# Optimization experiments

Hardware: AMD Instinct MI355X
Metric: run time of the kernel (lower is better)

Reference implementation:

```python
import jax, jax.numpy as jnp
import numpy as np

B, T, D = 2, 2048, 1024
HV, HK = 16, 8
DK, DV = 64, 64
K_DIM = HK * DK          # 512
V_DIM = HV * DV          # 1024
CONV_DIM = 2 * K_DIM + V_DIM  # 2048
KS = 4                   # short-conv kernel size
EPS = 1e-6               # rms_norm_eps / l2norm eps


def setup_inputs() -> dict:
    key = jax.random.key(0)
    ks = jax.random.split(key, 9)
    g = lambda k, shape, sc: (jax.random.normal(k, shape, jnp.float32) * sc)
    return {
        "hidden_states": g(ks[0], (B, T, D), 1.0),
        "W_qkv": g(ks[1], (D, CONV_DIM), 0.02),
        "W_z": g(ks[2], (D, V_DIM), 0.02),
        "W_b": g(ks[3], (D, HV), 0.02),
        "W_a": g(ks[4], (D, HV), 0.02),
        "dt_bias": jnp.ones((HV,), jnp.float32),
        "A_log": jnp.log(jax.random.uniform(ks[5], (HV,), jnp.float32, 1e-3, 16.0)),
        "conv_w": g(ks[6], (CONV_DIM, KS), 0.2),
        "norm_w": jnp.ones((DV,), jnp.float32),
        "W_out": g(ks[7], (V_DIM, D), 0.02),
    }


def _causal_conv_silu(x, w):
    # depthwise causal conv1d over time, followed by SiLU (FLA ShortConvolution default)
    # x: [B,T,C], w: [C,KS]
    xp = jnp.pad(x, ((0, 0), (KS - 1, 0), (0, 0)))
    y = sum(xp[:, i:i + x.shape[1], :] * w[:, i] for i in range(KS))
    return jax.nn.silu(y)


def _l2norm(x):
    return x * jax.lax.rsqrt(jnp.sum(x * x, -1, keepdims=True) + EPS)


def _forward(hidden_states, W_qkv, W_z, W_b, W_a, dt_bias, A_log, conv_w, norm_w, W_out):
    b_, t_ = hidden_states.shape[:2]
    mixed_qkv = hidden_states @ W_qkv                       # [B,T,conv_dim]
    z = (hidden_states @ W_z).reshape(b_, t_, HV, DV)       # gate branch
    beta = jax.nn.sigmoid(hidden_states @ W_b)              # [B,T,HV]
    g = -jnp.exp(A_log) * jax.nn.softplus(hidden_states @ W_a + dt_bias)  # [B,T,HV]

    mixed_qkv = _causal_conv_silu(mixed_qkv, conv_w)
    q, k, v = jnp.split(mixed_qkv, [K_DIM, 2 * K_DIM], axis=-1)
    q = q.reshape(b_, t_, HK, DK)
    k = k.reshape(b_, t_, HK, DK)
    v = v.reshape(b_, t_, HV, DV)
    # GQA expansion of q/k to the value-head count
    rep = HV // HK
    q = jnp.repeat(q, rep, axis=2)
    k = jnp.repeat(k, rep, axis=2)
    # l2-norm on q/k in kernel; q additionally scaled by 1/sqrt(dk)
    q = _l2norm(q) * (DK ** -0.5)
    k = _l2norm(k)

    # gated delta-rule recurrence over time (state S: [B,HV,DK,DV])
    qT = q.transpose(1, 0, 2, 3)
    kT = k.transpose(1, 0, 2, 3)
    vT = v.transpose(1, 0, 2, 3)
    gT = g.transpose(1, 0, 2)
    bT = beta.transpose(1, 0, 2)

    def step(S, xs):
        q_t, k_t, v_t, g_t, b_t = xs
        S = S * jnp.exp(g_t)[..., None, None]
        kv = jnp.einsum('bhk,bhkv->bhv', k_t, S)
        S = S + jnp.einsum('bhk,bhv->bhkv', k_t, (v_t - kv) * b_t[..., None])
        o_t = jnp.einsum('bhk,bhkv->bhv', q_t, S)
        return S, o_t

    S0 = jnp.zeros((b_, HV, DK, DV), jnp.float32)
    _, oT = jax.lax.scan(step, S0, (qT, kT, vT, gT, bT))
    o = oT.transpose(1, 0, 2, 3)                            # [B,T,HV,DV]

    # gated RMSNorm: rmsnorm(o) * weight * silu(z)
    var = jnp.mean(o * o, axis=-1, keepdims=True)
    o = o * jax.lax.rsqrt(var + EPS) * norm_w * jax.nn.silu(z)

    return o.reshape(b_, t_, V_DIM) @ W_out


def reference(hidden_states, W_qkv, W_z, W_b, W_a, dt_bias, A_log, conv_w, norm_w, W_out):
    return _forward(hidden_states, W_qkv, W_z, W_b, W_a, dt_bias, A_log, conv_w, norm_w, W_out)
```

## Files before the change

kernel.cpp:

```cpp
#include <hip/hip_runtime.h>
#include <hip/hip_bf16.h>


typedef unsigned short u16;
typedef float f32x4 __attribute__((ext_vector_type(4)));
typedef short bf16x8 __attribute__((ext_vector_type(8)));
typedef u16 u16x4 __attribute__((ext_vector_type(4)));
typedef const __attribute__((address_space(1))) void* gptr_t;
typedef __attribute__((address_space(3))) void* lptr_t;

#define B_    2
#define T_    2048
#define HV_   16
#define HK_   8
#define NC_   32
#define BT_   4096
#define QKVZ_ 3072
#define NCOL_ 3200

__device__ __forceinline__ u16 f2bf(float f) {
  return __builtin_bit_cast(u16, __float2bfloat16(f));
}
__device__ __forceinline__ float bf2f(u16 u) {
  return __bfloat162float(__builtin_bit_cast(__hip_bfloat16, u));
}
__device__ __forceinline__ float sigm(float x) { return 1.f / (1.f + __expf(-x)); }

__global__ __launch_bounds__(256) void k_cast_hs(const float* __restrict__ in,
                                                 u16* __restrict__ out) {
  int i = (blockIdx.x * 256 + threadIdx.x) * 4;
  float4 v = *(const float4*)(in + i);
  u16x4 o; o.x = f2bf(v.x); o.y = f2bf(v.y); o.z = f2bf(v.z); o.w = f2bf(v.w);
  *(u16x4*)(out + i) = o;
}

__global__ __launch_bounds__(256) void k_tcast(const float* __restrict__ src,
                                               u16* __restrict__ dst, int R, int C) {
  __shared__ float tile[32][33];
  int c0 = blockIdx.x * 32, r0 = blockIdx.y * 32;
  int cx = threadIdx.x & 31, ry = threadIdx.x >> 5;
#pragma unroll
  for (int j = 0; j < 4; ++j)
    tile[ry * 4 + j][cx] = src[(long)(r0 + ry * 4 + j) * C + c0 + cx];
  __syncthreads();
#pragma unroll
  for (int j = 0; j < 4; ++j)
    dst[(long)(c0 + ry * 4 + j) * R + r0 + cx] = f2bf(tile[cx][ry * 4 + j]);
}

__global__ __launch_bounds__(256) void k_wcatT(const float* __restrict__ Wqkv,
                                               const float* __restrict__ Wz,
                                               const float* __restrict__ Wb,
                                               const float* __restrict__ Wa,
                                               u16* __restrict__ dst) {
  __shared__ float tile[32][33];
  int n0 = blockIdx.x * 32, k0 = blockIdx.y * 32;
  int cx = threadIdx.x & 31, ry = threadIdx.x >> 5;
#pragma unroll
  for (int j = 0; j < 4; ++j) {
    int kk = k0 + ry * 4 + j;
    int n = n0 + cx;
    float v;
    if (n < 2048)      v = Wqkv[(long)kk * 2048 + n];
    else if (n < 3072) v = Wz[(long)kk * 1024 + (n - 2048)];
    else if (n < 3088) v = Wb[kk * 16 + (n - 3072)];
    else if (n < 3104) v = Wa[kk * 16 + (n - 3088)];
    else               v = 0.f;
    tile[ry * 4 + j][cx] = v;
  }
  __syncthreads();
#pragma unroll
  for (int j = 0; j < 4; ++j)
    dst[(long)(n0 + ry * 4 + j) * 1024 + k0 + cx] = f2bf(tile[cx][ry * 4 + j]);
}

__global__ __launch_bounds__(256) void k_gemm(const u16* __restrict__ A,
                                              const u16* __restrict__ Bt,
                                              u16* __restrict__ C0,
                                              float* __restrict__ C1,
                                              int M, int N, int K, int mode) {
  __shared__ u16 As[128 * 64];
  __shared__ u16 Bs[128 * 64];
  int tid = threadIdx.x;
  int wid = tid >> 6, lane = tid & 63;
  int row0 = blockIdx.y * 128, col0 = blockIdx.x * 128;
  int wr = wid >> 1, wc = wid & 1;
  f32x4 acc[4][4];
#pragma unroll
  for (int m = 0; m < 4; ++m)
#pragma unroll
    for (int n = 0; n < 4; ++n) acc[m][n] = (f32x4){0.f, 0.f, 0.f, 0.f};

  int srow = lane >> 3;
  int skoff = (lane & 7) * 8;

  for (int k0 = 0; k0 < K; k0 += 64) {
#pragma unroll
    for (int it = 0; it < 4; ++it) {
      int seg = wid * 4 + it;
      int r = seg * 8 + srow;
      const u16* gA = A + (long)(row0 + r) * K + k0 + skoff;
      const u16* gB = Bt + (long)(col0 + r) * K + k0 + skoff;
      __builtin_amdgcn_global_load_lds((gptr_t)gA, (lptr_t)(As + seg * 512), 16, 0, 0);
      __builtin_amdgcn_global_load_lds((gptr_t)gB, (lptr_t)(Bs + seg * 512), 16, 0, 0);
    }
    asm volatile("s_waitcnt vmcnt(0)" ::: "memory");
    __syncthreads();
#pragma unroll
    for (int ks = 0; ks < 2; ++ks) {
      bf16x8 af[4], bfr[4];
      int kk = ks * 32 + (lane >> 4) * 8;
      int rA = wr * 64 + (lane & 15);
      int rB = wc * 64 + (lane & 15);
#pragma unroll
      for (int m = 0; m < 4; ++m) af[m] = *(const bf16x8*)(As + (rA + m * 16) * 64 + kk);
#pragma unroll
      for (int n = 0; n < 4; ++n) bfr[n] = *(const bf16x8*)(Bs + (rB + n * 16) * 64 + kk);
#pragma unroll
      for (int m = 0; m < 4; ++m)
#pragma unroll
        for (int n = 0; n < 4; ++n)
          acc[m][n] = __builtin_amdgcn_mfma_f32_16x16x32_bf16(af[m], bfr[n], acc[m][n], 0, 0, 0);
    }
    __syncthreads();
  }
#pragma unroll
  for (int m = 0; m < 4; ++m)
#pragma unroll
    for (int n = 0; n < 4; ++n)
#pragma unroll
      for (int r = 0; r < 4; ++r) {
        int row = row0 + wr * 64 + m * 16 + (lane >> 4) * 4 + r;
        int col = col0 + wc * 64 + n * 16 + (lane & 15);
        float v = acc[m][n][r];
        if (mode == 0) {
          if (col < QKVZ_) C0[(long)row * QKVZ_ + col] = f2bf(v);
          else             C1[(long)row * 128 + (col - QKVZ_)] = v;
        } else {
          C1[(long)row * N + col] = v;
        }
      }
}

__global__ __launch_bounds__(64) void k_conv(const u16* __restrict__ qkvz,
                                             const float* __restrict__ ba,
                                             const float* __restrict__ convw,
                                             const float* __restrict__ Alog,
                                             const float* __restrict__ dtb,
                                             u16* __restrict__ qn, u16* __restrict__ kn,
                                             u16* __restrict__ vb,
                                             float* __restrict__ beta, float* __restrict__ gb) {
  int bt = blockIdx.x;
  int t = bt & 2047;
  int l = threadIdx.x;
  long rb = (long)bt * QKVZ_;
#pragma unroll 1
  for (int j = 0; j < 32; ++j) {
    int c = j * 64 + l;
    float4 w = *(const float4*)(convw + c * 4);
    float a = 0.f;
#pragma unroll
    for (int d = 0; d < 4; ++d) {
      int tt = t - 3 + d;
      float x = (tt >= 0) ? bf2f(qkvz[rb + (long)(tt - t) * QKVZ_ + c]) : 0.f;
      a += x * ((const float*)&w)[d];
    }
    float y = a * sigm(a);
    if (j < 16) {
      float ss = y * y;
#pragma unroll
      for (int m = 1; m < 64; m <<= 1) ss += __shfl_xor(ss, m);
      float sc = rsqrtf(ss + 1e-6f);
      if (j < 8) qn[((long)bt * 8 + j) * 64 + l] = f2bf(y * sc * 0.125f);
      else       kn[((long)bt * 8 + (j - 8)) * 64 + l] = f2bf(y * sc);
    } else {
      vb[((long)bt * 16 + (j - 16)) * 64 + l] = f2bf(y);
    }
  }
  if (l < 16) {
    float xb = ba[(long)bt * 128 + l];
    beta[bt * 16 + l] = sigm(xb);
    float xa = ba[(long)bt * 128 + 16 + l] + dtb[l];
    float sp = (xa > 20.f) ? xa : log1pf(__expf(xa));
    gb[bt * 16 + l] = -__expf(Alog[l]) * sp;
  }
}

__global__ __launch_bounds__(256) void k_cpk2(const u16* __restrict__ qn,
                                              const u16* __restrict__ kn,
                                              const u16* __restrict__ vb,
                                              const float* __restrict__ beta,
                                              const float* __restrict__ gb,
                                              float* __restrict__ Gbuf,
                                              u16* __restrict__ TKTb,
                                              u16* __restrict__ WlTb, u16* __restrict__ MTb,
                                              u16* __restrict__ Pb, u16* __restrict__ Bb) {
  int c = blockIdx.x, hv = blockIdx.y, b = blockIdx.z;
  int hk = hv >> 1;
  int bh = b * HV_ + hv;
  int tid = threadIdx.x;
  int wv = tid >> 6, lane = tid & 63;
  int frow = lane & 15, fk = (lane >> 4) * 8;

  __shared__ __align__(16) char smem[78848];
  u16* Ks   = (u16*)smem;
  u16* Qs   = (u16*)(smem + 9216);
  u16* Ktt  = Qs;
  u16* As_  = (u16*)(smem + 18432);
  u16* RHSt = (u16*)(smem + 27648);
  u16* Xt   = (u16*)(smem + 46080);
  u16* T4   = (u16*)(smem + 64512);
  u16* Yl   = (u16*)(smem + 68608);
  __shared__ float Gl[64];
  __shared__ float Bl[64];

  long tbase = (long)b * T_ + c * 64;
  long tile = ((long)bh * NC_ + c) * 4096;

  if (tid < 64) {
    Gl[tid] = gb[(tbase + tid) * HV_ + hv];
    Bl[tid] = beta[(tbase + tid) * HV_ + hv];
  }
  if (tid == 0) {
    float s = 0.f;
    for (int i = 0; i < 64; ++i) { s += Gl[i]; Gl[i] = s; }
  }
  if (tid < 64) Gbuf[((long)bh * NC_ + c) * 64 + tid] = Gl[tid];
  for (int e = tid; e < 4608; e += 256) ((float*)Xt)[e] = 0.f;
  for (int e = tid; e < 2560; e += 256) ((float*)Yl)[e] = 0.f;
  for (int e = tid; e < 4096; e += 256) {
    int i = e >> 6, k = e & 63;
    Ks[i * 72 + k] = kn[(tbase + i) * 512 + hk * 64 + k];
    Qs[i * 72 + k] = qn[(tbase + i) * 512 + hk * 64 + k];
  }
  __syncthreads();

  {
    bf16x8 aKs[2];
#pragma unroll
    for (int ks = 0; ks < 2; ++ks)
      aKs[ks] = *(const bf16x8*)&Ks[(wv * 16 + frow) * 72 + ks * 32 + fk];
    f32x4 accM[4], accA[4];
#pragma unroll
    for (int nt = 0; nt < 4; ++nt) { accM[nt] = (f32x4){0,0,0,0}; accA[nt] = (f32x4){0,0,0,0}; }
#pragma unroll
    for (int ks = 0; ks < 2; ++ks) {
#pragma unroll
      for (int nt = 0; nt < 4; ++nt) {
        bf16x8 bq = *(const bf16x8*)&Qs[(nt * 16 + frow) * 72 + ks * 32 + fk];
        bf16x8 bk = *(const bf16x8*)&Ks[(nt * 16 + frow) * 72 + ks * 32 + fk];
        accM[nt] = __builtin_amdgcn_mfma_f32_16x16x32_bf16(aKs[ks], bq, accM[nt], 0, 0, 0);
        accA[nt] = __builtin_amdgcn_mfma_f32_16x16x32_bf16(aKs[ks], bk, accA[nt], 0, 0, 0);
      }
    }
#pragma unroll
    for (int nt = 0; nt < 4; ++nt) {
      int i = nt * 16 + frow;
#pragma unroll
      for (int r = 0; r < 4; ++r) {
        int s = wv * 16 + (lane >> 4) * 4 + r;
        float val = (s <= i) ? accM[nt][r] * __expf(Gl[i] - Gl[s]) : 0.f;
        MTb[tile + s * 64 + i] = f2bf(val);
      }
    }
#pragma unroll
    for (int nt = 0; nt < 4; ++nt) {
      int s = nt * 16 + frow;
#pragma unroll
      for (int r = 0; r < 4; ++r) {
        int i = wv * 16 + (lane >> 4) * 4 + r;
        float val = (s < i) ? Bl[i] * __expf(Gl[i] - Gl[s]) * accA[nt][r] : 0.f;
        As_[i * 72 + s] = f2bf(val);
      }
    }
  }

  for (int e = tid; e < 4096; e += 256) {
    int i = e >> 6, v = e & 63;
    RHSt[v * 72 + i] = f2bf(Bl[i] * bf2f(vb[(tbase + i) * 1024 + hv * 64 + v]));
  }
  for (int e = tid; e < 4096; e += 256) {
    int i = e >> 6, k = e & 63;
    RHSt[(64 + k) * 72 + i] = f2bf(Bl[i] * __expf(Gl[i]) * bf2f(Ks[i * 72 + k]));
  }
  __syncthreads();

  {
    if (lane < 16) {
      int cc = lane;
      float Tc[16];
#pragma unroll
      for (int j = 0; j < 16; ++j) Tc[j] = (j == cc) ? 1.f : 0.f;
#pragma unroll
      for (int s = 0; s < 15; ++s)
#pragma unroll
        for (int i = s + 1; i < 16; ++i) {
          float a = bf2f(As_[(wv * 16 + i) * 72 + wv * 16 + s]);
          Tc[i] -= a * Tc[s];
        }
#pragma unroll
      for (int i = 0; i < 16; ++i) T4[(wv * 16 + i) * 32 + cc] = f2bf(Tc[i]);
    } else if (lane < 32) {
      int c2 = lane - 16;
#pragma unroll
      for (int i = 0; i < 16; ++i) T4[(wv * 16 + i) * 32 + 16 + c2] = 0;
    }
  }
  __syncthreads();

#pragma unroll 1
  for (int bb = 0; bb < 4; ++bb) {
    f32x4 uacc[2];
    uacc[0] = (f32x4){0,0,0,0}; uacc[1] = (f32x4){0,0,0,0};
#pragma unroll
    for (int ks = 0; ks < 2; ++ks) {
      bf16x8 bfr = *(const bf16x8*)&As_[(bb * 16 + frow) * 72 + ks * 32 + fk];
#pragma unroll
      for (int mt = 0; mt < 2; ++mt) {
        bf16x8 aa = *(const bf16x8*)&Xt[((wv * 2 + mt) * 16 + frow) * 72 + ks * 32 + fk];
        uacc[mt] = __builtin_amdgcn_mfma_f32_16x16x32_bf16(aa, bfr, uacc[mt], 0, 0, 0);
      }
    }
#pragma unroll
    for (int mt = 0; mt < 2; ++mt)
#pragma unroll
      for (int r = 0; r < 4; ++r) {
        int vr = (wv * 2 + mt) * 16 + (lane >> 4) * 4 + r;
        float y = bf2f(RHSt[vr * 72 + bb * 16 + frow]) - uacc[mt][r];
        Yl[vr * 40 + frow] = f2bf(y);
      }
    __syncthreads();
    {
      bf16x8 tb = *(const bf16x8*)&T4[(bb * 16 + frow) * 32 + fk];
      f32x4 zacc[2];
      zacc[0] = (f32x4){0,0,0,0}; zacc[1] = (f32x4){0,0,0,0};
#pragma unroll
      for (int mt = 0; mt < 2; ++mt) {
        bf16x8 aa = *(const bf16x8*)&Yl[((wv * 2 + mt) * 16 + frow) * 40 + fk];
        zacc[mt] = __builtin_amdgcn_mfma_f32_16x16x32_bf16(aa, tb, zacc[mt], 0, 0, 0);
      }
#pragma unroll
      for (int mt = 0; mt < 2; ++mt)
#pragma unroll
        for (int r = 0; r < 4; ++r) {
          int vr = (wv * 2 + mt) * 16 + (lane >> 4) * 4 + r;
          Xt[vr * 72 + bb * 16 + frow] = f2bf(zacc[mt][r]);
        }
    }
    __syncthreads();
  }

  float gend = Gl[63];
  for (int e = tid; e < 4096; e += 256) {
    int i = e >> 6, r = e & 63;
    Ktt[r * 72 + i] = f2bf(__expf(gend - Gl[i]) * bf2f(Ks[i * 72 + r]));
  }
#pragma unroll
  for (int t8 = 0; t8 < 2; ++t8) {
    int seg = tid + t8 * 256;
    int row = seg >> 2, s4 = (seg & 3) * 16;
    bf16x8 x0 = *(const bf16x8*)&Xt[row * 72 + s4];
    bf16x8 x1 = *(const bf16x8*)&Xt[row * 72 + s4 + 8];
    u16* dst = (row < 64) ? (WlTb + tile + row * 64 + s4)
                          : (TKTb + tile + (long)(row - 64) * 64 + s4);
    *(bf16x8*)dst = x0;
    *(bf16x8*)(dst + 8) = x1;
  }
  __syncthreads();

  {
    f32x4 acc[4];
#pragma unroll
    for (int nt = 0; nt < 4; ++nt) acc[nt] = (f32x4){0,0,0,0};
#pragma unroll
    for (int ks = 0; ks < 2; ++ks) {
      bf16x8 aa = *(const bf16x8*)&Ktt[(wv * 16 + frow) * 72 + ks * 32 + fk];
#pragma unroll
      for (int nt = 0; nt < 4; ++nt) {
        bf16x8 bfr = *(const bf16x8*)&Xt[(nt * 16 + frow) * 72 + ks * 32 + fk];
        acc[nt] = __builtin_amdgcn_mfma_f32_16x16x32_bf16(aa, bfr, acc[nt], 0, 0, 0);
      }
    }
#pragma unroll
    for (int nt = 0; nt < 4; ++nt) {
      int v = nt * 16 + frow;
#pragma unroll
      for (int r = 0; r < 4; ++r) {
        int rr = wv * 16 + (lane >> 4) * 4 + r;
        Bb[tile + rr * 64 + v] = f2bf(acc[nt][r]);
      }
    }
  }
  {
    f32x4 acc[4];
#pragma unroll
    for (int nt = 0; nt < 4; ++nt) acc[nt] = (f32x4){0,0,0,0};
#pragma unroll
    for (int ks = 0; ks < 2; ++ks) {
      bf16x8 aa = *(const bf16x8*)&Xt[(64 + wv * 16 + frow) * 72 + ks * 32 + fk];
#pragma unroll
      for (int nt = 0; nt < 4; ++nt) {
        bf16x8 bfr = *(const bf16x8*)&Ktt[(nt * 16 + frow) * 72 + ks * 32 + fk];
        acc[nt] = __builtin_amdgcn_mfma_f32_16x16x32_bf16(aa, bfr, acc[nt], 0, 0, 0);
      }
    }
#pragma unroll
    for (int nt = 0; nt < 4; ++nt) {
      int rr = nt * 16 + frow;
#pragma unroll
      for (int r = 0; r < 4; ++r) {
        int k2 = wv * 16 + (lane >> 4) * 4 + r;
        Pb[tile + k2 * 64 + rr] = f2bf(acc[nt][r]);
      }
    }
  }
}

__global__ __launch_bounds__(256) void k_seq2(const u16* __restrict__ Pb,
                                              const u16* __restrict__ Bb,
                                              const float* __restrict__ Gbuf,
                                              u16* __restrict__ Stb) {
  int vblk = blockIdx.x, bh = blockIdx.y;
  int tid = threadIdx.x;
  __shared__ u16 Abf[2][4096];
  __shared__ u16 Bbf[2][512];
  __shared__ float S_lds[64][10];
  __shared__ float gam[NC_];
  int i_ = tid & 63, vg = tid >> 6;
  int wv = tid >> 6, ln = tid & 63;
  if (tid < NC_) gam[tid] = __expf(Gbuf[((long)bh * NC_ + tid) * 64 + 63]);
  for (int e = tid; e < 640; e += 256) ((float*)S_lds)[e] = 0.f;
  float a0 = 0.f, a1 = 0.f;
  {
    long tl = (long)bh * NC_ * 4096;
    const u16* gA = Pb + tl + wv * 512 + ln * 8;
    __builtin_amdgcn_global_load_lds((gptr_t)gA, (lptr_t)&Abf[0][wv * 512], 16, 0, 0);
    __builtin_amdgcn_global_load_lds((gptr_t)(gA + 2048), (lptr_t)&Abf[0][2048 + wv * 512], 16, 0, 0);
    int ii = tid >> 2, vp = tid & 3;
    const u16* gB = Bb + tl + ii * 64 + vblk * 8 + vp * 2;
    __builtin_amdgcn_global_load_lds((gptr_t)gB, (lptr_t)&Bbf[0][wv * 128], 4, 0, 0);
  }
  for (int c = 0; c < NC_; ++c) {
    int cur = c & 1;
    asm volatile("s_waitcnt vmcnt(0)" ::: "memory");
    __syncthreads();
    if (c + 1 < NC_) {
      long tl = ((long)bh * NC_ + c + 1) * 4096;
      const u16* gA = Pb + tl + wv * 512 + ln * 8;
      __builtin_amdgcn_global_load_lds((gptr_t)gA, (lptr_t)&Abf[cur ^ 1][wv * 512], 16, 0, 0);
      __builtin_amdgcn_global_load_lds((gptr_t)(gA + 2048), (lptr_t)&Abf[cur ^ 1][2048 + wv * 512], 16, 0, 0);
      int ii = tid >> 2, vp = tid & 3;
      const u16* gB = Bb + tl + ii * 64 + vblk * 8 + vp * 2;
      __builtin_amdgcn_global_load_lds((gptr_t)gB, (lptr_t)&Bbf[cur ^ 1][wv * 128], 4, 0, 0);
    }
    {
      long stile = ((long)bh * NC_ + c) * 4096;
      int v0 = vblk * 8 + vg * 2;
      Stb[stile + (long)v0 * 64 + i_] = f2bf(a0);
      Stb[stile + (long)(v0 + 1) * 64 + i_] = f2bf(a1);
    }
    float g = gam[c];
    float n0 = 0.f, n1 = 0.f;
#pragma unroll 8
    for (int k = 0; k < 64; ++k) {
      float p = bf2f(Abf[cur][k * 64 + i_]);
      float2 sv = *(const float2*)&S_lds[k][vg * 2];
      n0 += p * sv.x;
      n1 += p * sv.y;
    }
    float b0 = bf2f(Bbf[cur][i_ * 8 + vg * 2]);
    float b1 = bf2f(Bbf[cur][i_ * 8 + vg * 2 + 1]);
    a0 = g * a0 - n0 + b0;
    a1 = g * a1 - n1 + b1;
    __syncthreads();
    S_lds[i_][vg * 2] = a0;
    S_lds[i_][vg * 2 + 1] = a1;
  }
}

__global__ __launch_bounds__(256) void k_ok2(const u16* __restrict__ MTb,
                                             const u16* __restrict__ TKTb,
                                             const u16* __restrict__ WlTb,
                                             const u16* __restrict__ Stb,
                                             const u16* __restrict__ qn,
                                             const float* __restrict__ Gbuf,
                                             float* __restrict__ O) {
  int c = blockIdx.x, hv = blockIdx.y, b = blockIdx.z;
  int bh = b * HV_ + hv, hk = hv >> 1;
  int tid = threadIdx.x;
  __shared__ float TKt[64][68];
  __shared__ float Ss[64][68];
  __shared__ float Ws[64][68];
  __shared__ float Qt[64][68];
  __shared__ float Gl[64];
  long tile = ((long)bh * NC_ + c) * 4096;
  long tbase = (long)b * T_ + c * 64;
  if (tid < 64) Gl[tid] = Gbuf[((long)bh * NC_ + c) * 64 + tid];
  __syncthreads();
  for (int e = tid; e < 4096; e += 256)
    TKt[e >> 6][e & 63] = bf2f(TKTb[tile + e]);
  for (int e = tid; e < 4096; e += 256) {
    int i = e >> 6, k = e & 63;
    Qt[k][i] = __expf(Gl[i]) * bf2f(qn[(tbase + i) * 512 + hk * 64 + k]);
  }
  for (int e = tid; e < 4096; e += 256) {
    int v = e >> 6, x = e & 63;
    Ss[x][v] = bf2f(Stb[tile + e]);
    Ws[x][v] = bf2f(WlTb[tile + e]);
  }
  __syncthreads();
  int tx = tid & 15, ty = tid >> 4;
  int i0 = ty * 4, v0 = tx * 4;
  float w[4][4];
#pragma unroll
  for (int r = 0; r < 4; ++r) *(f32x4*)w[r] = *(const f32x4*)&Ws[i0 + r][v0];
  for (int k = 0; k < 64; ++k) {
    f32x4 tk = *(const f32x4*)&TKt[k][i0];
    f32x4 sv = *(const f32x4*)&Ss[k][v0];
#pragma unroll
    for (int r = 0; r < 4; ++r)
#pragma unroll
      for (int q = 0; q < 4; ++q) w[r][q] -= tk[r] * sv[q];
  }
  __syncthreads();
#pragma unroll
  for (int r = 0; r < 4; ++r) *(f32x4*)&Ws[i0 + r][v0] = *(const f32x4*)w[r];
  for (int e = tid; e < 4096; e += 256)
    TKt[e >> 6][e & 63] = bf2f(MTb[tile + e]);
  __syncthreads();
  float o[4][4] = {};
  for (int s = 0; s < 64; ++s) {
    f32x4 mv = *(const f32x4*)&TKt[s][i0];
    f32x4 wv = *(const f32x4*)&Ws[s][v0];
#pragma unroll
    for (int r = 0; r < 4; ++r)
#pragma unroll
      for (int q = 0; q < 4; ++q) o[r][q] += mv[r] * wv[q];
  }
  for (int k = 0; k < 64; ++k) {
    f32x4 qv = *(const f32x4*)&Qt[k][i0];
    f32x4 sv = *(const f32x4*)&Ss[k][v0];
#pragma unroll
    for (int r = 0; r < 4; ++r)
#pragma unroll
      for (int q = 0; q < 4; ++q) o[r][q] += qv[r] * sv[q];
  }
#pragma unroll
  for (int r = 0; r < 4; ++r) {
    float4 o4 = make_float4(o[r][0], o[r][1], o[r][2], o[r][3]);
    *(float4*)&O[((tbase + i0 + r) * HV_ + hv) * 64 + v0] = o4;
  }
}

__global__ __launch_bounds__(256) void k_rms(const float* __restrict__ O,
                                             const u16* __restrict__ qkvz,
                                             const float* __restrict__ normw,
                                             u16* __restrict__ on) {
  int bt = blockIdx.x;
  int tid = threadIdx.x;
  __shared__ float ps[256];
  __shared__ float rstd[16];
  float4 o4 = *(const float4*)&O[(long)bt * 1024 + tid * 4];
  ps[tid] = o4.x * o4.x + o4.y * o4.y + o4.z * o4.z + o4.w * o4.w;
  __syncthreads();
  if (tid < 16) {
    float s = 0.f;
#pragma unroll
    for (int u = 0; u < 16; ++u) s += ps[tid * 16 + u];
    rstd[tid] = rsqrtf(s * (1.f / 64.f) + 1e-6f);
  }
  __syncthreads();
  float rs = rstd[tid >> 4];
  u16x4 ov;
#pragma unroll
  for (int j = 0; j < 4; ++j) {
    int idx = tid * 4 + j;
    float z = bf2f(qkvz[(long)bt * QKVZ_ + 2048 + idx]);
    float val = ((const float*)&o4)[j] * rs * normw[idx & 63] * (z * sigm(z));
    ((u16*)&ov)[j] = f2bf(val);
  }
  *(u16x4*)(on + (long)bt * 1024 + tid * 4) = ov;
}

extern "C" void kernel_launch(void* const* d_in, const int* in_sizes, int n_in,
                              void* d_out, int out_size, void* d_ws, size_t ws_size,
                              hipStream_t stream) {
  const float* hs    = (const float*)d_in[0];
  const float* Wqkv  = (const float*)d_in[1];
  const float* Wz    = (const float*)d_in[2];
  const float* Wb    = (const float*)d_in[3];
  const float* Wa    = (const float*)d_in[4];
  const float* dtb   = (const float*)d_in[5];
  const float* Alog  = (const float*)d_in[6];
  const float* convw = (const float*)d_in[7];
  const float* normw = (const float*)d_in[8];
  const float* Wout  = (const float*)d_in[9];
  float* out = (float*)d_out;

  char* p = (char*)d_ws;
  auto take = [&](size_t bytes) {
    char* q = p;
    p += (bytes + 255) & ~(size_t)255;
    return (void*)q;
  };
  u16*   qkvz  = (u16*)take((size_t)BT_ * QKVZ_ * 2);
  float* ba    = (float*)take((size_t)BT_ * 128 * 4);
  u16*   hsb   = (u16*)take((size_t)BT_ * 1024 * 2);
  u16*   wcatT = (u16*)take((size_t)NCOL_ * 1024 * 2);
  u16*   woutT = (u16*)take((size_t)1024 * 1024 * 2);
  u16*   qn    = (u16*)take((size_t)BT_ * 512 * 2);
  u16*   kn    = (u16*)take((size_t)BT_ * 512 * 2);
  u16*   vbuf  = (u16*)take((size_t)BT_ * 1024 * 2);
  float* beta  = (float*)take((size_t)BT_ * 16 * 4);
  float* gbuf  = (float*)take((size_t)BT_ * 16 * 4);
  float* Gcum  = (float*)take((size_t)1024 * 64 * 4);
  u16*   TKTb  = (u16*)take((size_t)1024 * 4096 * 2);
  u16*   WlTb  = (u16*)take((size_t)1024 * 4096 * 2);
  u16*   MTb   = (u16*)take((size_t)1024 * 4096 * 2);
  u16*   Pb    = (u16*)take((size_t)1024 * 4096 * 2);
  u16*   Bb    = (u16*)take((size_t)1024 * 4096 * 2);
  u16*   Stb   = (u16*)take((size_t)1024 * 4096 * 2);
  float* Obuf  = (float*)take((size_t)BT_ * 1024 * 4);
  u16*   onb   = (u16*)take((size_t)BT_ * 1024 * 2);

  k_cast_hs<<<dim3(4096), dim3(256), 0, stream>>>(hs, hsb);
  k_wcatT<<<dim3(100, 32), dim3(256), 0, stream>>>(Wqkv, Wz, Wb, Wa, wcatT);
  k_tcast<<<dim3(32, 32), dim3(256), 0, stream>>>(Wout, woutT, 1024, 1024);
  k_gemm<<<dim3(25, 32), dim3(256), 0, stream>>>(hsb, wcatT, qkvz, ba, 4096, NCOL_, 1024, 0);
  k_conv<<<dim3(4096), dim3(64), 0, stream>>>(qkvz, ba, convw, Alog, dtb, qn, kn, vbuf, beta, gbuf);
  k_cpk2<<<dim3(32, 16, 2), dim3(256), 0, stream>>>(qn, kn, vbuf, beta, gbuf, Gcum, TKTb, WlTb, MTb, Pb, Bb);
  k_seq2<<<dim3(8, 32), dim3(256), 0, stream>>>(Pb, Bb, Gcum, Stb);
  k_ok2<<<dim3(32, 16, 2), dim3(256), 0, stream>>>(MTb, TKTb, WlTb, Stb, qn, Gcum, Obuf);
  k_rms<<<dim3(4096), dim3(256), 0, stream>>>(Obuf, qkvz, normw, onb);
  k_gemm<<<dim3(8, 32), dim3(256), 0, stream>>>(onb, woutT, (u16*)nullptr, out, 4096, 1024, 1024, 1);
}
```

Before: 363.0 us.

## Add pipelined 256x256 input GEMM, vectorize conv, move chunk output to MFMA

Replaces the input projection GEMM with a 512-thread 256x256-tile kernel. It uses a 4-stage global_load_lds pipeline with swizzled LDS and setprio around the MFMAs, and pads the weight columns to 3328. The conv kernel now handles 8 channels per thread with vector bf16 loads, and its l2norm reduction needs only 3 shuffles. The chunk output kernel drops its fp32 scalar outer products for bf16 MFMA, with the M/TK intermediate layouts changed to match. The risks are bf16 rounding of the intermediate W and Q tiles and lower occupancy in the big GEMM.

Result: faster. 291.9 us (-19.6%).

```diff
diff --git a/kernel.cpp b/kernel.cpp
--- a/kernel.cpp
+++ b/kernel.cpp
@@ -16,7 +16,7 @@
 #define NC_   32
 #define BT_   4096
 #define QKVZ_ 3072
-#define NCOL_ 3200
+#define NPAD_ 3328
 
 __device__ __forceinline__ u16 f2bf(float f) {
   return __builtin_bit_cast(u16, __float2bfloat16(f));
@@ -74,11 +74,101 @@
     dst[(long)(n0 + ry * 4 + j) * 1024 + k0 + cx] = f2bf(tile[cx][ry * 4 + j]);
 }
 
+__global__ __launch_bounds__(512, 1) void k_g1(const u16* __restrict__ A,
+                                               const u16* __restrict__ Bt,
+                                               u16* __restrict__ C0,
+                                               float* __restrict__ C1) {
+  extern __shared__ u16 smem[];
+  const int K = 1024;
+  int tid = threadIdx.x;
+  int wv = tid >> 6, lane = tid & 63;
+  int wm = wv >> 2, wn = wv & 3;
+  int frow = lane & 15, kq = lane >> 4;
+  long row0 = blockIdx.y * 256, col0 = blockIdx.x * 256;
+
+  f32x4 acc[8][4];
+#pragma unroll
+  for (int m = 0; m < 8; ++m)
+#pragma unroll
+    for (int n = 0; n < 4; ++n) acc[m][n] = (f32x4){0.f, 0.f, 0.f, 0.f};
+
+  int lr = lane >> 2;
+  int kc_src = ((lane & 3) - (lane >> 3)) & 3;
+
+  auto stage = [&](int ts) {
+#pragma unroll
+    for (int op = 0; op < 2; ++op) {
+      u16* base = smem + op * 32768 + (ts & 3) * 8192;
+      const u16* gsrc = op ? Bt : A;
+      long grow0 = op ? col0 : row0;
+#pragma unroll
+      for (int it = 0; it < 2; ++it) {
+        int seg = wv * 2 + it;
+        const u16* g = gsrc + (grow0 + seg * 16 + lr) * K + ts * 32 + kc_src * 8;
+        __builtin_amdgcn_global_load_lds((gptr_t)g, (lptr_t)(base + seg * 512), 16, 0, 0);
+      }
+    }
+  };
+
+  auto section = [&](int h) {
+    const char* Ab = (const char*)(smem + (h & 3) * 8192);
+    const char* Bb = (const char*)(smem + 32768 + (h & 3) * 8192);
+    bf16x8 af[8], bfr[4];
+#pragma unroll
+    for (int mt = 0; mt < 8; ++mt) {
+      int R = wm * 128 + mt * 16 + frow;
+      af[mt] = *(const bf16x8*)(Ab + R * 64 + (((kq + (R >> 1)) & 3) << 4));
+    }
+#pragma unroll
+    for (int nt = 0; nt < 4; ++nt) {
+      int R = wn * 64 + nt * 16 + frow;
+      bfr[nt] = *(const bf16x8*)(Bb + R * 64 + (((kq + (R >> 1)) & 3) << 4));
+    }
+    __builtin_amdgcn_s_setprio(1);
+#pragma unroll
+    for (int mt = 0; mt < 8; ++mt)
+#pragma unroll
+      for (int nt = 0; nt < 4; ++nt)
+        acc[mt][nt] = __builtin_amdgcn_mfma_f32_16x16x32_bf16(af[mt], bfr[nt], acc[mt][nt], 0, 0, 0);
+    __builtin_amdgcn_s_setprio(0);
+  };
+
+  stage(0); stage(1); stage(2);
+#pragma unroll 1
+  for (int h = 0; h < 29; ++h) {
+    asm volatile("s_waitcnt vmcnt(8)" ::: "memory");
+    __syncthreads();
+    stage(h + 3);
+    section(h);
+  }
+  asm volatile("s_waitcnt vmcnt(8)" ::: "memory");
+  __syncthreads();
+  section(29);
+  asm volatile("s_waitcnt vmcnt(4)" ::: "memory");
+  __syncthreads();
+  section(30);
+  asm volatile("s_waitcnt vmcnt(0)" ::: "memory");
+  __syncthreads();
+  section(31);
+
+#pragma unroll
+  for (int m = 0; m < 8; ++m)
+#pragma unroll
+    for (int n = 0; n < 4; ++n)
+#pragma unroll
+      for (int r = 0; r < 4; ++r) {
+        long row = row0 + wm * 128 + m * 16 + kq * 4 + r;
+        long col = col0 + wn * 64 + n * 16 + frow;
+        float v = acc[m][n][r];
+        if (col < QKVZ_)      C0[row * QKVZ_ + col] = f2bf(v);
+        else if (col < 3200)  C1[row * 128 + (col - QKVZ_)] = v;
+      }
+}
+
 __global__ __launch_bounds__(256) void k_gemm(const u16* __restrict__ A,
                                               const u16* __restrict__ Bt,
-                                              u16* __restrict__ C0,
                                               float* __restrict__ C1,
-                                              int M, int N, int K, int mode) {
+                                              int M, int N, int K) {
   __shared__ u16 As[128 * 64];
   __shared__ u16 Bs[128 * 64];
   int tid = threadIdx.x;
@@ -90,10 +180,8 @@
   for (int m = 0; m < 4; ++m)
 #pragma unroll
     for (int n = 0; n < 4; ++n) acc[m][n] = (f32x4){0.f, 0.f, 0.f, 0.f};
-
   int srow = lane >> 3;
   int skoff = (lane & 7) * 8;
-
   for (int k0 = 0; k0 < K; k0 += 64) {
 #pragma unroll
     for (int it = 0; it < 4; ++it) {
@@ -132,57 +220,68 @@
       for (int r = 0; r < 4; ++r) {
         int row = row0 + wr * 64 + m * 16 + (lane >> 4) * 4 + r;
         int col = col0 + wc * 64 + n * 16 + (lane & 15);
-        float v = acc[m][n][r];
-        if (mode == 0) {
-          if (col < QKVZ_) C0[(long)row * QKVZ_ + col] = f2bf(v);
-          else             C1[(long)row * 128 + (col - QKVZ_)] = v;
-        } else {
-          C1[(long)row * N + col] = v;
-        }
-      }
-}
-
-__global__ __launch_bounds__(64) void k_conv(const u16* __restrict__ qkvz,
-                                             const float* __restrict__ ba,
-                                             const float* __restrict__ convw,
-                                             const float* __restrict__ Alog,
-                                             const float* __restrict__ dtb,
-                                             u16* __restrict__ qn, u16* __restrict__ kn,
-                                             u16* __restrict__ vb,
-                                             float* __restrict__ beta, float* __restrict__ gb) {
+        C1[(long)row * N + col] = acc[m][n][r];
+      }
+}
+
+__global__ __launch_bounds__(256) void k_conv(const u16* __restrict__ qkvz,
+                                              const float* __restrict__ ba,
+                                              const float* __restrict__ convw,
+                                              const float* __restrict__ Alog,
+                                              const float* __restrict__ dtb,
+                                              u16* __restrict__ qn, u16* __restrict__ kn,
+                                              u16* __restrict__ vb,
+                                              float* __restrict__ beta, float* __restrict__ gb) {
   int bt = blockIdx.x;
   int t = bt & 2047;
-  int l = threadIdx.x;
+  int g = threadIdx.x;
+  int c = g * 8;
   long rb = (long)bt * QKVZ_;
-#pragma unroll 1
-  for (int j = 0; j < 32; ++j) {
-    int c = j * 64 + l;
-    float4 w = *(const float4*)(convw + c * 4);
+  bf16x8 x[4];
+#pragma unroll
+  for (int d = 0; d < 4; ++d) {
+    int tt = t - 3 + d;
+    if (tt >= 0) x[d] = *(const bf16x8*)(qkvz + rb + (long)(d - 3) * QKVZ_ + c);
+    else         x[d] = (bf16x8){0, 0, 0, 0, 0, 0, 0, 0};
+  }
+  float y[8];
+#pragma unroll
+  for (int j = 0; j < 8; ++j) {
+    float4 w4 = *(const float4*)(convw + (c + j) * 4);
     float a = 0.f;
 #pragma unroll
     for (int d = 0; d < 4; ++d) {
       int tt = t - 3 + d;
-      float x = (tt >= 0) ? bf2f(qkvz[rb + (long)(tt - t) * QKVZ_ + c]) : 0.f;
-      a += x * ((const float*)&w)[d];
-    }
-    float y = a * sigm(a);
-    if (j < 16) {
-      float ss = y * y;
-#pragma unroll
-      for (int m = 1; m < 64; m <<= 1) ss += __shfl_xor(ss, m);
-      float sc = rsqrtf(ss + 1e-6f);
-      if (j < 8) qn[((long)bt * 8 + j) * 64 + l] = f2bf(y * sc * 0.125f);
-      else       kn[((long)bt * 8 + (j - 8)) * 64 + l] = f2bf(y * sc);
-    } else {
-      vb[((long)bt * 16 + (j - 16)) * 64 + l] = f2bf(y);
-    }
-  }
-  if (l < 16) {
-    float xb = ba[(long)bt * 128 + l];
-    beta[bt * 16 + l] = sigm(xb);
-    float xa = ba[(long)bt * 128 + 16 + l] + dtb[l];
+      float xv = (tt >= 0) ? bf2f((u16)x[d][j]) : 0.f;
+      a += xv * ((const float*)&w4)[d];
+    }
+    y[j] = a * sigm(a);
+  }
+  bf16x8 o;
+  if (g < 128) {
+    float ss = 0.f;
+#pragma unroll
+    for (int j = 0; j < 8; ++j) ss += y[j] * y[j];
+    ss += __shfl_xor(ss, 1);
+    ss += __shfl_xor(ss, 2);
+    ss += __shfl_xor(ss, 4);
+    float sc = rsqrtf(ss + 1e-6f);
+    if (g < 64) sc *= 0.125f;
+#pragma unroll
+    for (int j = 0; j < 8; ++j) ((u16*)&o)[j] = f2bf(y[j] * sc);
+    if (g < 64) *(bf16x8*)(qn + (long)bt * 512 + c) = o;
+    else        *(bf16x8*)(kn + (long)bt * 512 + (c - 512)) = o;
+  } else {
+#pragma unroll
+    for (int j = 0; j < 8; ++j) ((u16*)&o)[j] = f2bf(y[j]);
+    *(bf16x8*)(vb + (long)bt * 1024 + (c - 1024)) = o;
+  }
+  if (g < 16) {
+    float xb = ba[(long)bt * 128 + g];
+    beta[bt * 16 + g] = sigm(xb);
+    float xa = ba[(long)bt * 128 + 16 + g] + dtb[g];
     float sp = (xa > 20.f) ? xa : log1pf(__expf(xa));
-    gb[bt * 16 + l] = -__expf(Alog[l]) * sp;
+    gb[bt * 16 + g] = -__expf(Alog[g]) * sp;
   }
 }
 
@@ -192,8 +291,8 @@
                                               const float* __restrict__ beta,
                                               const float* __restrict__ gb,
                                               float* __restrict__ Gbuf,
-                                              u16* __restrict__ TKTb,
-                                              u16* __restrict__ WlTb, u16* __restrict__ MTb,
+                                              u16* __restrict__ TKb,
+                                              u16* __restrict__ WlTb, u16* __restrict__ Mb,
                                               u16* __restrict__ Pb, u16* __restrict__ Bb) {
   int c = blockIdx.x, hv = blockIdx.y, b = blockIdx.z;
   int hk = hv >> 1;
@@ -236,10 +335,12 @@
   __syncthreads();
 
   {
-    bf16x8 aKs[2];
-#pragma unroll
-    for (int ks = 0; ks < 2; ++ks)
+    bf16x8 aKs[2], aQs[2];
+#pragma unroll
+    for (int ks = 0; ks < 2; ++ks) {
       aKs[ks] = *(const bf16x8*)&Ks[(wv * 16 + frow) * 72 + ks * 32 + fk];
+      aQs[ks] = *(const bf16x8*)&Qs[(wv * 16 + frow) * 72 + ks * 32 + fk];
+    }
     f32x4 accM[4], accA[4];
 #pragma unroll
     for (int nt = 0; nt < 4; ++nt) { accM[nt] = (f32x4){0,0,0,0}; accA[nt] = (f32x4){0,0,0,0}; }
@@ -247,20 +348,19 @@
     for (int ks = 0; ks < 2; ++ks) {
 #pragma unroll
       for (int nt = 0; nt < 4; ++nt) {
-        bf16x8 bq = *(const bf16x8*)&Qs[(nt * 16 + frow) * 72 + ks * 32 + fk];
         bf16x8 bk = *(const bf16x8*)&Ks[(nt * 16 + frow) * 72 + ks * 32 + fk];
-        accM[nt] = __builtin_amdgcn_mfma_f32_16x16x32_bf16(aKs[ks], bq, accM[nt], 0, 0, 0);
+        accM[nt] = __builtin_amdgcn_mfma_f32_16x16x32_bf16(aQs[ks], bk, accM[nt], 0, 0, 0);
         accA[nt] = __builtin_amdgcn_mfma_f32_16x16x32_bf16(aKs[ks], bk, accA[nt], 0, 0, 0);
       }
     }
 #pragma unroll
     for (int nt = 0; nt < 4; ++nt) {
-      int i = nt * 16 + frow;
-#pragma unroll
-      for (int r = 0; r < 4; ++r) {
-        int s = wv * 16 + (lane >> 4) * 4 + r;
+      int s = nt * 16 + frow;
+#pragma unroll
+      for (int r = 0; r < 4; ++r) {
+        int i = wv * 16 + (lane >> 4) * 4 + r;
         float val = (s <= i) ? accM[nt][r] * __expf(Gl[i] - Gl[s]) : 0.f;
-        MTb[tile + s * 64 + i] = f2bf(val);
+        Mb[tile + i * 64 + s] = f2bf(val);
       }
     }
 #pragma unroll
@@ -356,15 +456,17 @@
     Ktt[r * 72 + i] = f2bf(__expf(gend - Gl[i]) * bf2f(Ks[i * 72 + r]));
   }
 #pragma unroll
-  for (int t8 = 0; t8 < 2; ++t8) {
-    int seg = tid + t8 * 256;
+  for (int t8 = 0; t8 < 1; ++t8) {
+    int seg = tid;
     int row = seg >> 2, s4 = (seg & 3) * 16;
     bf16x8 x0 = *(const bf16x8*)&Xt[row * 72 + s4];
     bf16x8 x1 = *(const bf16x8*)&Xt[row * 72 + s4 + 8];
-    u16* dst = (row < 64) ? (WlTb + tile + row * 64 + s4)
-                          : (TKTb + tile + (long)(row - 64) * 64 + s4);
-    *(bf16x8*)dst = x0;
-    *(bf16x8*)(dst + 8) = x1;
+    *(bf16x8*)(WlTb + tile + row * 64 + s4) = x0;
+    *(bf16x8*)(WlTb + tile + row * 64 + s4 + 8) = x1;
+  }
+  for (int e = tid; e < 4096; e += 256) {
+    int i = e >> 6, k = e & 63;
+    TKb[tile + e] = Xt[(64 + k) * 72 + i];
   }
   __syncthreads();
 
@@ -478,8 +580,8 @@
   }
 }
 
-__global__ __launch_bounds__(256) void k_ok2(const u16* __restrict__ MTb,
-                                             const u16* __restrict__ TKTb,
+__global__ __launch_bounds__(256) void k_ok3(const u16* __restrict__ Mb,
+                                             const u16* __restrict__ TKb,
                                              const u16* __restrict__ WlTb,
                                              const u16* __restrict__ Stb,
                                              const u16* __restrict__ qn,
@@ -488,67 +590,84 @@
   int c = blockIdx.x, hv = blockIdx.y, b = blockIdx.z;
   int bh = b * HV_ + hv, hk = hv >> 1;
   int tid = threadIdx.x;
-  __shared__ float TKt[64][68];
-  __shared__ float Ss[64][68];
-  __shared__ float Ws[64][68];
-  __shared__ float Qt[64][68];
+  int wv = tid >> 6, lane = tid & 63;
+  int frow = lane & 15, fk = (lane >> 4) * 8;
+  __shared__ __align__(16) u16 St[64 * 72];
+  __shared__ __align__(16) u16 TKr[64 * 72];
+  __shared__ __align__(16) u16 Wl_[64 * 72];
+  __shared__ __align__(16) u16 Qh[64 * 72];
   __shared__ float Gl[64];
   long tile = ((long)bh * NC_ + c) * 4096;
   long tbase = (long)b * T_ + c * 64;
   if (tid < 64) Gl[tid] = Gbuf[((long)bh * NC_ + c) * 64 + tid];
-  __syncthreads();
-  for (int e = tid; e < 4096; e += 256)
-    TKt[e >> 6][e & 63] = bf2f(TKTb[tile + e]);
+  bf16x8 mreg[2];
+#pragma unroll
+  for (int j = 0; j < 2; ++j) mreg[j] = *(const bf16x8*)(Mb + tile + tid * 16 + j * 8);
+  __syncthreads();
   for (int e = tid; e < 4096; e += 256) {
-    int i = e >> 6, k = e & 63;
-    Qt[k][i] = __expf(Gl[i]) * bf2f(qn[(tbase + i) * 512 + hk * 64 + k]);
-  }
-  for (int e = tid; e < 4096; e += 256) {
-    int v = e >> 6, x = e & 63;
-    Ss[x][v] = bf2f(Stb[tile + e]);
-    Ws[x][v] = bf2f(WlTb[tile + e]);
-  }
-  __syncthreads();
-  int tx = tid & 15, ty = tid >> 4;
-  int i0 = ty * 4, v0 = tx * 4;
-  float w[4][4];
-#pragma unroll
-  for (int r = 0; r < 4; ++r) *(f32x4*)w[r] = *(const f32x4*)&Ws[i0 + r][v0];
-  for (int k = 0; k < 64; ++k) {
-    f32x4 tk = *(const f32x4*)&TKt[k][i0];
-    f32x4 sv = *(const f32x4*)&Ss[k][v0];
-#pragma unroll
-    for (int r = 0; r < 4; ++r)
-#pragma unroll
-      for (int q = 0; q < 4; ++q) w[r][q] -= tk[r] * sv[q];
-  }
-  __syncthreads();
-#pragma unroll
-  for (int r = 0; r < 4; ++r) *(f32x4*)&Ws[i0 + r][v0] = *(const f32x4*)w[r];
-  for (int e = tid; e < 4096; e += 256)
-    TKt[e >> 6][e & 63] = bf2f(MTb[tile + e]);
-  __syncthreads();
-  float o[4][4] = {};
-  for (int s = 0; s < 64; ++s) {
-    f32x4 mv = *(const f32x4*)&TKt[s][i0];
-    f32x4 wv = *(const f32x4*)&Ws[s][v0];
-#pragma unroll
-    for (int r = 0; r < 4; ++r)
-#pragma unroll
-      for (int q = 0; q < 4; ++q) o[r][q] += mv[r] * wv[q];
-  }
-  for (int k = 0; k < 64; ++k) {
-    f32x4 qv = *(const f32x4*)&Qt[k][i0];
-    f32x4 sv = *(const f32x4*)&Ss[k][v0];
-#pragma unroll
-    for (int r = 0; r < 4; ++r)
-#pragma unroll
-      for (int q = 0; q < 4; ++q) o[r][q] += qv[r] * sv[q];
-  }
-#pragma unroll
-  for (int r = 0; r < 4; ++r) {
-    float4 o4 = make_float4(o[r][0], o[r][1], o[r][2], o[r][3]);
-    *(float4*)&O[((tbase + i0 + r) * HV_ + hv) * 64 + v0] = o4;
+    int r = e >> 6, x = e & 63;
+    St[r * 72 + x] = Stb[tile + e];
+    TKr[r * 72 + x] = TKb[tile + e];
+    Wl_[r * 72 + x] = WlTb[tile + e];
+    Qh[r * 72 + x] = f2bf(__expf(Gl[r]) * bf2f(qn[(tbase + r) * 512 + hk * 64 + x]));
+  }
+  __syncthreads();
+  {
+    f32x4 acc1[4];
+#pragma unroll
+    for (int nt = 0; nt < 4; ++nt) acc1[nt] = (f32x4){0,0,0,0};
+#pragma unroll
+    for (int ks = 0; ks < 2; ++ks) {
+      bf16x8 aa = *(const bf16x8*)&St[(wv * 16 + frow) * 72 + ks * 32 + fk];
+#pragma unroll
+      for (int nt = 0; nt < 4; ++nt) {
+        bf16x8 bb2 = *(const bf16x8*)&TKr[(nt * 16 + frow) * 72 + ks * 32 + fk];
+        acc1[nt] = __builtin_amdgcn_mfma_f32_16x16x32_bf16(aa, bb2, acc1[nt], 0, 0, 0);
+      }
+    }
+#pragma unroll
+    for (int nt = 0; nt < 4; ++nt) {
+      int i = nt * 16 + frow;
+#pragma unroll
+      for (int r = 0; r < 4; ++r) {
+        int v = wv * 16 + (lane >> 4) * 4 + r;
+        float wt = bf2f(Wl_[v * 72 + i]) - acc1[nt][r];
+        Wl_[v * 72 + i] = f2bf(wt);
+      }
+    }
+  }
+  __syncthreads();
+#pragma unroll
+  for (int j = 0; j < 2; ++j) {
+    int e = tid * 16 + j * 8;
+    *(bf16x8*)&TKr[(e >> 6) * 72 + (e & 63)] = mreg[j];
+  }
+  __syncthreads();
+  {
+    f32x4 acc2[4];
+#pragma unroll
+    for (int nt = 0; nt < 4; ++nt) acc2[nt] = (f32x4){0,0,0,0};
+#pragma unroll
+    for (int ks = 0; ks < 2; ++ks) {
+      bf16x8 am = *(const bf16x8*)&TKr[(wv * 16 + frow) * 72 + ks * 32 + fk];
+      bf16x8 aq = *(const bf16x8*)&Qh[(wv * 16 + frow) * 72 + ks * 32 + fk];
+#pragma unroll
+      for (int nt = 0; nt < 4; ++nt) {
+        bf16x8 bw = *(const bf16x8*)&Wl_[(nt * 16 + frow) * 72 + ks * 32 + fk];
+        bf16x8 bs = *(const bf16x8*)&St[(nt * 16 + frow) * 72 + ks * 32 + fk];
+        acc2[nt] = __builtin_amdgcn_mfma_f32_16x16x32_bf16(am, bw, acc2[nt], 0, 0, 0);
+        acc2[nt] = __builtin_amdgcn_mfma_f32_16x16x32_bf16(aq, bs, acc2[nt], 0, 0, 0);
+      }
+    }
+#pragma unroll
+    for (int nt = 0; nt < 4; ++nt) {
+      int v = nt * 16 + frow;
+#pragma unroll
+      for (int r = 0; r < 4; ++r) {
+        int i = wv * 16 + (lane >> 4) * 4 + r;
+        O[((tbase + i) * HV_ + hv) * 64 + v] = acc2[nt][r];
+      }
+    }
   }
 }
 
@@ -606,7 +725,7 @@
   u16*   qkvz  = (u16*)take((size_t)BT_ * QKVZ_ * 2);
   float* ba    = (float*)take((size_t)BT_ * 128 * 4);
   u16*   hsb   = (u16*)take((size_t)BT_ * 1024 * 2);
-  u16*   wcatT = (u16*)take((size_t)NCOL_ * 1024 * 2);
+  u16*   wcatT = (u16*)take((size_t)NPAD_ * 1024 * 2);
   u16*   woutT = (u16*)take((size_t)1024 * 1024 * 2);
   u16*   qn    = (u16*)take((size_t)BT_ * 512 * 2);
   u16*   kn    = (u16*)take((size_t)BT_ * 512 * 2);
@@ -614,9 +733,9 @@
   float* beta  = (float*)take((size_t)BT_ * 16 * 4);
   float* gbuf  = (float*)take((size_t)BT_ * 16 * 4);
   float* Gcum  = (float*)take((size_t)1024 * 64 * 4);
-  u16*   TKTb  = (u16*)take((size_t)1024 * 4096 * 2);
+  u16*   TKb   = (u16*)take((size_t)1024 * 4096 * 2);
   u16*   WlTb  = (u16*)take((size_t)1024 * 4096 * 2);
-  u16*   MTb   = (u16*)take((size_t)1024 * 4096 * 2);
+  u16*   Mb    = (u16*)take((size_t)1024 * 4096 * 2);
   u16*   Pb    = (u16*)take((size_t)1024 * 4096 * 2);
   u16*   Bb    = (u16*)take((size_t)1024 * 4096 * 2);
   u16*   Stb   = (u16*)take((size_t)1024 * 4096 * 2);
@@ -624,13 +743,13 @@
   u16*   onb   = (u16*)take((size_t)BT_ * 1024 * 2);
 
   k_cast_hs<<<dim3(4096), dim3(256), 0, stream>>>(hs, hsb);
-  k_wcatT<<<dim3(100, 32), dim3(256), 0, stream>>>(Wqkv, Wz, Wb, Wa, wcatT);
+  k_wcatT<<<dim3(104, 32), dim3(256), 0, stream>>>(Wqkv, Wz, Wb, Wa, wcatT);
   k_tcast<<<dim3(32, 32), dim3(256), 0, stream>>>(Wout, woutT, 1024, 1024);
-  k_gemm<<<dim3(25, 32), dim3(256), 0, stream>>>(hsb, wcatT, qkvz, ba, 4096, NCOL_, 1024, 0);
-  k_conv<<<dim3(4096), dim3(64), 0, stream>>>(qkvz, ba, convw, Alog, dtb, qn, kn, vbuf, beta, gbuf);
-  k_cpk2<<<dim3(32, 16, 2), dim3(256), 0, stream>>>(qn, kn, vbuf, beta, gbuf, Gcum, TKTb, WlTb, MTb, Pb, Bb);
+  k_g1<<<dim3(13, 16), dim3(512), 131072, stream>>>(hsb, wcatT, qkvz, ba);
+  k_conv<<<dim3(4096), dim3(256), 0, stream>>>(qkvz, ba, convw, Alog, dtb, qn, kn, vbuf, beta, gbuf);
+  k_cpk2<<<dim3(32, 16, 2), dim3(256), 0, stream>>>(qn, kn, vbuf, beta, gbuf, Gcum, TKb, WlTb, Mb, Pb, Bb);
   k_seq2<<<dim3(8, 32), dim3(256), 0, stream>>>(Pb, Bb, Gcum, Stb);
-  k_ok2<<<dim3(32, 16, 2), dim3(256), 0, stream>>>(MTb, TKTb, WlTb, Stb, qn, Gcum, Obuf);
+  k_ok3<<<dim3(32, 16, 2), dim3(256), 0, stream>>>(Mb, TKb, WlTb, Stb, qn, Gcum, Obuf);
   k_rms<<<dim3(4096), dim3(256), 0, stream>>>(Obuf, qkvz, normw, onb);
-  k_gemm<<<dim3(8, 32), dim3(256), 0, stream>>>(onb, woutT, (u16*)nullptr, out, 4096, 1024, 1024, 1);
-}
+  k_gemm<<<dim3(8, 32), dim3(256), 0, stream>>>(onb, woutT, out, 4096, 1024, 1024);
+}
```
